# Performance work log

Measured on AMD Instinct MI355X. Metric: run time of the kernel, lower is better.

The kernel has to match this reference:

```python
import jax, jax.numpy as jnp
import numpy as np

PAD = 0
N_SENSE = 3
VOCAB = 100000
OUT_VOCAB = 50000
D = 128
B = 64
MAX_LEN = 512


def setup_inputs() -> dict:
    key = jax.random.key(0)
    ks = jax.random.split(key, 8)
    inputs = jax.random.randint(ks[0], (B, MAX_LEN * N_SENSE), 0, VOCAB, dtype=jnp.int64 if jax.config.jax_enable_x64 else jnp.int32)
    length_weights = jax.random.uniform(ks[1], (B, 1, 1), dtype=jnp.float32, minval=0.1, maxval=1.0)
    word_attn_mask = jax.random.bernoulli(ks[2], 0.1, (B, MAX_LEN))
    embedding = jax.random.normal(ks[3], (VOCAB, D), dtype=jnp.float32) * 0.02
    W_attn = jax.random.normal(ks[4], (1, D), dtype=jnp.float32) * 0.02
    b_attn = jnp.zeros((1,), dtype=jnp.float32)
    W_lin = jax.random.normal(ks[5], (OUT_VOCAB, D), dtype=jnp.float32) * 0.02
    b_lin = jnp.zeros((OUT_VOCAB,), dtype=jnp.float32)
    return {"inputs": inputs, "length_weights": length_weights, "word_attn_mask": word_attn_mask,
            "embedding": embedding, "W_attn": W_attn, "b_attn": b_attn, "W_lin": W_lin, "b_lin": b_lin}


def reference(inputs, length_weights, word_attn_mask, embedding, W_attn, b_attn, W_lin, b_lin):
    Bsz, LS = inputs.shape
    L = LS // N_SENSE
    # padding row contributes zeros (nn.Embedding padding_idx=PAD)
    E = embedding.at[PAD].set(0.0)
    embeds = E[inputs]                                   # [B, L*S, D]
    embeds4 = embeds.reshape(Bsz, L, N_SENSE, -1)
    embed_mean = embeds4.mean(axis=2)                    # [B, L, D]
    # word-level attention: Linear(D,1) -> mask -> softmax over words
    word_imp = jnp.einsum('bld,d->bl', embed_mean, W_attn[0]) + b_attn[0]
    word_imp = jnp.where(word_attn_mask, -jnp.inf, word_imp)
    word_w = jax.nn.softmax(word_imp, axis=-1)           # [B, L]
    context = jnp.einsum('bl,bld->bd', word_w, embed_mean)  # [B, D]
    # sense-level attention: similarity of each sense embedding to context
    sim = jnp.einsum('bnd,bd->bn', embeds, context)      # [B, L*S]
    sense_w = jax.nn.softmax(sim.reshape(Bsz, L, N_SENSE), axis=-1).reshape(Bsz, LS)
    attn_w = length_weights.reshape(Bsz, 1) * sense_w    # scale by 1/length
    attn_w = jnp.where(inputs == PAD, 0.0, attn_w)
    hidden = jnp.einsum('bn,bnd->bd', attn_w, embeds)    # [B, D]
    logits = hidden @ W_lin.T + b_lin                    # [B, OUT_VOCAB]
    return jax.nn.log_softmax(logits, axis=-1)
```

## Files before the change

### kernel.cpp

```cpp
#include <hip/hip_runtime.h>
#include <math.h>

#define B_    64
#define L_    512
#define S_    3
#define D_    128
#define OV_   50000
#define VOC_  100000
#define NBLK_ 782

typedef __attribute__((ext_vector_type(8))) short bf16x8;
typedef __attribute__((ext_vector_type(4))) float f32x4;

__device__ __forceinline__ float waveReduceSum(float v) {
#pragma unroll
    for (int off = 32; off >= 1; off >>= 1) v += __shfl_xor(v, off, 64);
    return v;
}
__device__ __forceinline__ float waveReduceMax(float v) {
#pragma unroll
    for (int off = 32; off >= 1; off >>= 1) v = fmaxf(v, __shfl_xor(v, off, 64));
    return v;
}

__device__ __forceinline__ short f2bf(float f) {
    unsigned int u = __float_as_uint(f);
    return (short)((u + 0x7FFFu + ((u >> 16) & 1u)) >> 16);
}

__global__ __launch_bounds__(256) void prequery_kernel(
    const float* __restrict__ emb, const float* __restrict__ Wa,
    float* __restrict__ P, float* __restrict__ context,
    float* __restrict__ hidden)
{
    const int tid = threadIdx.x;
    if (blockIdx.x < 64 && tid < D_) {
        context[blockIdx.x * D_ + tid] = 0.f;
        hidden[blockIdx.x * D_ + tid]  = 0.f;
    }

    const int lane = tid & 63;
    const int q = lane >> 4;
    const int j = lane & 15;
    const int waveg = blockIdx.x * 4 + (tid >> 6);
    const int nwaves = gridDim.x * 4;

    const float4 wa0 = ((const float4*)Wa)[2 * j];
    const float4 wa1 = ((const float4*)Wa)[2 * j + 1];

    for (int r0 = waveg * 4; r0 < VOC_; r0 += nwaves * 4) {
        const float4* row = (const float4*)(emb + (long)(r0 + q) * D_ + j * 8);
        float4 e0 = row[0], e1 = row[1];
        float s = e0.x * wa0.x + e0.y * wa0.y + e0.z * wa0.z + e0.w * wa0.w
                + e1.x * wa1.x + e1.y * wa1.y + e1.z * wa1.z + e1.w * wa1.w;
#pragma unroll
        for (int off = 8; off >= 1; off >>= 1) s += __shfl_xor(s, off, 64);
        if (j == 0) P[r0 + q] = s;
    }
}

__global__ __launch_bounds__(256) void context_kernel(
    const int* __restrict__ inputs, const int* __restrict__ mask,
    const float* __restrict__ P, const float* __restrict__ ba,
    const float* __restrict__ emb, float* __restrict__ context)
{
    const int b    = blockIdx.x >> 4;
    const int base = (blockIdx.x & 15) * 32;
    const int tid  = threadIdx.x;
    const int wave = tid >> 6, lane = tid & 63;
    const int h = lane >> 5, j = lane & 31;

    __shared__ float s_imp[L_];
    __shared__ float s_red[4];
    __shared__ float s_part[8][D_];

    const int* in_b = inputs + b * (L_ * S_);
    const float babias = ba[0];

#pragma unroll
    for (int half = 0; half < 2; ++half) {
        const int l = tid + half * 256;
        float acc = 0.f;
#pragma unroll
        for (int s = 0; s < S_; ++s) {
            int idx = in_b[l * S_ + s];
            if (idx != 0) acc += P[idx];
        }
        float imp = acc * (1.0f / 3.0f) + babias;
        s_imp[l] = mask[b * L_ + l] ? -INFINITY : imp;
    }
    __syncthreads();

    float v0 = s_imp[tid], v1 = s_imp[tid + 256];
    float m = waveReduceMax(fmaxf(v0, v1));
    if (lane == 0) s_red[wave] = m;
    __syncthreads();
    m = fmaxf(fmaxf(s_red[0], s_red[1]), fmaxf(s_red[2], s_red[3]));
    __syncthreads();
    float p0 = expf(v0 - m), p1 = expf(v1 - m);
    float ssum = waveReduceSum(p0 + p1);
    if (lane == 0) s_red[wave] = ssum;
    __syncthreads();
    float inv = (1.0f / 3.0f) / (s_red[0] + s_red[1] + s_red[2] + s_red[3]);
    s_imp[tid]       = p0 * inv;
    s_imp[tid + 256] = p1 * inv;
    __syncthreads();

    float4 c = make_float4(0.f, 0.f, 0.f, 0.f);
    for (int wp = wave; wp < 16; wp += 4) {
        const int l = base + wp * 2 + h;
        const float w = s_imp[l];
        float4 mm = make_float4(0.f, 0.f, 0.f, 0.f);
#pragma unroll
        for (int s = 0; s < S_; ++s) {
            int idx = in_b[l * S_ + s];
            if (idx != 0) {
                float4 e = ((const float4*)(emb + (long)idx * D_))[j];
                mm.x += e.x; mm.y += e.y; mm.z += e.z; mm.w += e.w;
            }
        }
        c.x += w * mm.x; c.y += w * mm.y; c.z += w * mm.z; c.w += w * mm.w;
    }
    ((float4*)s_part[wave * 2 + h])[j] = c;
    __syncthreads();
    if (tid < D_) {
        float acc = 0.f;
#pragma unroll
        for (int p = 0; p < 8; ++p) acc += s_part[p][tid];
        atomicAdd(&context[b * D_ + tid], acc);
    }
}

__global__ __launch_bounds__(256) void sense_kernel(
    const int* __restrict__ inputs, const float* __restrict__ lwp,
    const float* __restrict__ context, const float* __restrict__ emb,
    float* __restrict__ hidden)
{
    const int b    = blockIdx.x >> 4;
    const int base = (blockIdx.x & 15) * 32;
    const int tid  = threadIdx.x;
    const int wave = tid >> 6, lane = tid & 63;
    const int h = lane >> 5, j = lane & 31;

    __shared__ float s_part[8][D_];

    const int* in_b = inputs + b * (L_ * S_);
    const float lwb = lwp[b];
    const float4 c4 = ((const float4*)(context + b * D_))[j];

    float4 hacc = make_float4(0.f, 0.f, 0.f, 0.f);

    for (int wp = wave; wp < 16; wp += 4) {
        const int l = base + wp * 2 + h;
        float4 e[S_]; int id[S_]; float sim[S_];
#pragma unroll
        for (int s = 0; s < S_; ++s) {
            id[s] = in_b[l * S_ + s];
            if (id[s] != 0) e[s] = ((const float4*)(emb + (long)id[s] * D_))[j];
            else e[s] = make_float4(0.f, 0.f, 0.f, 0.f);
            sim[s] = e[s].x * c4.x + e[s].y * c4.y + e[s].z * c4.z + e[s].w * c4.w;
        }
#pragma unroll
        for (int off = 16; off >= 1; off >>= 1) {
            sim[0] += __shfl_xor(sim[0], off, 64);
            sim[1] += __shfl_xor(sim[1], off, 64);
            sim[2] += __shfl_xor(sim[2], off, 64);
        }
        float e0 = expf(sim[0]), e1 = expf(sim[1]), e2 = expf(sim[2]);
        float f = lwb / (e0 + e1 + e2);
        float w0 = (id[0] != 0) ? e0 * f : 0.f;
        float w1 = (id[1] != 0) ? e1 * f : 0.f;
        float w2 = (id[2] != 0) ? e2 * f : 0.f;
        hacc.x += w0 * e[0].x + w1 * e[1].x + w2 * e[2].x;
        hacc.y += w0 * e[0].y + w1 * e[1].y + w2 * e[2].y;
        hacc.z += w0 * e[0].z + w1 * e[1].z + w2 * e[2].z;
        hacc.w += w0 * e[0].w + w1 * e[1].w + w2 * e[2].w;
    }
    ((float4*)s_part[wave * 2 + h])[j] = hacc;
    __syncthreads();
    if (tid < D_) {
        float acc = 0.f;
#pragma unroll
        for (int p = 0; p < 8; ++p) acc += s_part[p][tid];
        atomicAdd(&hidden[b * D_ + tid], acc);
    }
}

__global__ __launch_bounds__(256) void logits_kernel(
    const float* __restrict__ hidden, const float* __restrict__ Wl,
    const float* __restrict__ bl, float* __restrict__ logits,
    float* __restrict__ pS)
{
    __shared__ short s_hbf[64][136];
    const int tid  = threadIdx.x;
    const int wave = tid >> 6, lane = tid & 63;
    const int m15  = lane & 15, quad = lane >> 4;
    const int v    = blockIdx.x * 64 + wave * 16 + m15;
    const bool valid = (v < OV_);
    const int vc   = valid ? v : (OV_ - 1);

    for (int i = tid; i < 2048; i += 256) {
        float4 x = ((const float4*)hidden)[i];
        const int r = i >> 5;
        const int c = (i & 31) * 4;
        short* dst = &s_hbf[r][c];
        dst[0] = f2bf(x.x); dst[1] = f2bf(x.y);
        dst[2] = f2bf(x.z); dst[3] = f2bf(x.w);
    }
    __syncthreads();

    f32x4 acc[4];
#pragma unroll
    for (int t = 0; t < 4; ++t) acc[t] = (f32x4){0.f, 0.f, 0.f, 0.f};

    const float* wrow = Wl + (long)vc * D_ + quad * 8;
#pragma unroll
    for (int ks = 0; ks < 4; ++ks) {
        float4 x0 = *(const float4*)(wrow + ks * 32);
        float4 x1 = *(const float4*)(wrow + ks * 32 + 4);
        bf16x8 bfr;
        bfr[0] = f2bf(x0.x); bfr[1] = f2bf(x0.y); bfr[2] = f2bf(x0.z); bfr[3] = f2bf(x0.w);
        bfr[4] = f2bf(x1.x); bfr[5] = f2bf(x1.y); bfr[6] = f2bf(x1.z); bfr[7] = f2bf(x1.w);
#pragma unroll
        for (int t = 0; t < 4; ++t) {
            bf16x8 afr = *(const bf16x8*)&s_hbf[t * 16 + m15][ks * 32 + quad * 8];
            acc[t] = __builtin_amdgcn_mfma_f32_16x16x32_bf16(afr, bfr,
                                                             acc[t], 0, 0, 0);
        }
    }

    const float bias = bl[vc];
    if (valid) {
#pragma unroll
        for (int t = 0; t < 4; ++t)
#pragma unroll
            for (int r = 0; r < 4; ++r) {
                const int row = t * 16 + quad * 4 + r;
                logits[(long)row * OV_ + v] = acc[t][r] + bias;
            }
    }

    __shared__ float s_ps[64][4];
#pragma unroll
    for (int t = 0; t < 4; ++t) {
#pragma unroll
        for (int r = 0; r < 4; ++r) {
            float se = valid ? expf(acc[t][r] + bias) : 0.f;
#pragma unroll
            for (int off = 8; off >= 1; off >>= 1) se += __shfl_xor(se, off, 64);
            if (m15 == 0) s_ps[t * 16 + quad * 4 + r][wave] = se;
        }
    }
    __syncthreads();
    if (tid < 64)
        pS[tid * NBLK_ + blockIdx.x] = s_ps[tid][0] + s_ps[tid][1]
                                     + s_ps[tid][2] + s_ps[tid][3];
}

__global__ __launch_bounds__(256) void reducez_kernel(
    const float* __restrict__ pS, float* __restrict__ logZ)
{
    const int b = blockIdx.x;
    const int tid = threadIdx.x;
    const int wave = tid >> 6, lane = tid & 63;
    const float* rs = pS + b * NBLK_;
    __shared__ float s_red[4];

    float s = 0.f;
    for (int i = tid; i < NBLK_; i += 256) s += rs[i];
    s = waveReduceSum(s);
    if (lane == 0) s_red[wave] = s;
    __syncthreads();
    if (tid == 0)
        logZ[b] = logf(s_red[0] + s_red[1] + s_red[2] + s_red[3]);
}

__global__ __launch_bounds__(256) void finalize_kernel(
    const float* __restrict__ logits, const float* __restrict__ logZ,
    float* __restrict__ out)
{
    const long i4 = (long)blockIdx.x * 256 + threadIdx.x;
    const long e  = i4 * 4;
    const int b = (int)(e / OV_);
    const float z = logZ[b];
    float4 x = ((const float4*)logits)[i4];
    x.x -= z; x.y -= z; x.z -= z; x.w -= z;
    ((float4*)out)[i4] = x;
}

extern "C" void kernel_launch(void* const* d_in, const int* in_sizes, int n_in,
                              void* d_out, int out_size, void* d_ws, size_t ws_size,
                              hipStream_t stream) {
    const int*   inputs = (const int*)d_in[0];
    const float* lw     = (const float*)d_in[1];
    const int*   mask   = (const int*)d_in[2];
    const float* emb    = (const float*)d_in[3];
    const float* Wa     = (const float*)d_in[4];
    const float* ba     = (const float*)d_in[5];
    const float* Wl     = (const float*)d_in[6];
    const float* bl     = (const float*)d_in[7];
    float* out = (float*)d_out;

    float* ws = (float*)d_ws;
    float* hidden  = ws;
    float* logZ    = ws + 8192;
    float* logits  = ws + 8256;
    float* P       = logits + (long)B_ * OV_;
    float* context = P + VOC_;
    float* pS      = context + B_ * D_;

    prequery_kernel<<<625, 256, 0, stream>>>(emb, Wa, P, context, hidden);
    context_kernel<<<B_ * 16, 256, 0, stream>>>(inputs, mask, P, ba, emb, context);
    sense_kernel<<<B_ * 16, 256, 0, stream>>>(inputs, lw, context, emb, hidden);
    logits_kernel<<<NBLK_, 256, 0, stream>>>(hidden, Wl, bl, logits, pS);
    reducez_kernel<<<B_, 256, 0, stream>>>(pS, logZ);
    finalize_kernel<<<(B_ * OV_) / (4 * 256), 256, 0, stream>>>(logits, logZ, out);
}
```

Baseline: 161.0 us.

## Fuse attention and logits stages into cooperative kernels with grid sync

```diff
diff --git a/kernel.cpp b/kernel.cpp
--- a/kernel.cpp
+++ b/kernel.cpp
@@ -1,5 +1,8 @@
 #include <hip/hip_runtime.h>
+#include <hip/hip_cooperative_groups.h>
 #include <math.h>
+
+namespace cg = cooperative_groups;
 
 #define B_    64
 #define L_    512
@@ -31,13 +34,14 @@
 __global__ __launch_bounds__(256) void prequery_kernel(
     const float* __restrict__ emb, const float* __restrict__ Wa,
     float* __restrict__ P, float* __restrict__ context,
-    float* __restrict__ hidden)
+    float* __restrict__ hidden, float* __restrict__ rowsum)
 {
     const int tid = threadIdx.x;
     if (blockIdx.x < 64 && tid < D_) {
         context[blockIdx.x * D_ + tid] = 0.f;
         hidden[blockIdx.x * D_ + tid]  = 0.f;
     }
+    if (blockIdx.x == 64 && tid < B_) rowsum[tid] = 0.f;
 
     const int lane = tid & 63;
     const int q = lane >> 4;
@@ -59,6 +63,136 @@
     }
 }
 
+__device__ __forceinline__ void word_softmax(
+    const int* in_b, const int* __restrict__ mask, const float* __restrict__ P,
+    float babias, int b, float* s_imp, float* s_red)
+{
+    const int tid = threadIdx.x;
+    const int wave = tid >> 6, lane = tid & 63;
+#pragma unroll
+    for (int half = 0; half < 2; ++half) {
+        const int l = tid + half * 256;
+        float acc = 0.f;
+#pragma unroll
+        for (int s = 0; s < S_; ++s) {
+            int idx = in_b[l * S_ + s];
+            if (idx != 0) acc += P[idx];
+        }
+        float imp = acc * (1.0f / 3.0f) + babias;
+        s_imp[l] = mask[b * L_ + l] ? -INFINITY : imp;
+    }
+    __syncthreads();
+
+    float v0 = s_imp[tid], v1 = s_imp[tid + 256];
+    float m = waveReduceMax(fmaxf(v0, v1));
+    if (lane == 0) s_red[wave] = m;
+    __syncthreads();
+    m = fmaxf(fmaxf(s_red[0], s_red[1]), fmaxf(s_red[2], s_red[3]));
+    __syncthreads();
+    float p0 = expf(v0 - m), p1 = expf(v1 - m);
+    float ssum = waveReduceSum(p0 + p1);
+    if (lane == 0) s_red[wave] = ssum;
+    __syncthreads();
+    float inv = (1.0f / 3.0f) / (s_red[0] + s_red[1] + s_red[2] + s_red[3]);
+    s_imp[tid]       = p0 * inv;
+    s_imp[tid + 256] = p1 * inv;
+    __syncthreads();
+}
+
+__global__ __launch_bounds__(256, 2) void attn_fused(
+    const int* __restrict__ inputs, const int* __restrict__ mask,
+    const float* __restrict__ P, const float* __restrict__ ba,
+    const float* __restrict__ emb, const float* __restrict__ lwp,
+    float* __restrict__ context, float* __restrict__ hidden)
+{
+    cg::grid_group grid = cg::this_grid();
+
+    const int b    = blockIdx.x >> 3;
+    const int base = (blockIdx.x & 7) * 64;
+    const int tid  = threadIdx.x;
+    const int wave = tid >> 6, lane = tid & 63;
+    const int h = lane >> 5, j = lane & 31;
+
+    __shared__ float s_imp[L_];
+    __shared__ float s_red[4];
+    __shared__ float s_part[8][D_];
+
+    const int* in_b = inputs + b * (L_ * S_);
+    word_softmax(in_b, mask, P, ba[0], b, s_imp, s_red);
+
+    float4 ereg[8][3];
+    int    pmask[8];
+    float4 c = make_float4(0.f, 0.f, 0.f, 0.f);
+#pragma unroll
+    for (int it = 0; it < 8; ++it) {
+        const int l = base + (wave + it * 4) * 2 + h;
+        const float w = s_imp[l];
+        int pm = 0;
+        float4 mm = make_float4(0.f, 0.f, 0.f, 0.f);
+#pragma unroll
+        for (int s = 0; s < S_; ++s) {
+            int idx = in_b[l * S_ + s];
+            float4 e = make_float4(0.f, 0.f, 0.f, 0.f);
+            if (idx != 0) {
+                e = ((const float4*)(emb + (long)idx * D_))[j];
+                pm |= (1 << s);
+            }
+            ereg[it][s] = e;
+            mm.x += e.x; mm.y += e.y; mm.z += e.z; mm.w += e.w;
+        }
+        pmask[it] = pm;
+        c.x += w * mm.x; c.y += w * mm.y; c.z += w * mm.z; c.w += w * mm.w;
+    }
+    ((float4*)s_part[wave * 2 + h])[j] = c;
+    __syncthreads();
+    if (tid < D_) {
+        float acc = 0.f;
+#pragma unroll
+        for (int p = 0; p < 8; ++p) acc += s_part[p][tid];
+        atomicAdd(&context[b * D_ + tid], acc);
+    }
+
+    grid.sync();
+
+    const float lwb = lwp[b];
+    const float4 c4 = ((const float4*)(context + b * D_))[j];
+
+    float4 hacc = make_float4(0.f, 0.f, 0.f, 0.f);
+#pragma unroll
+    for (int it = 0; it < 8; ++it) {
+        float sim[S_];
+#pragma unroll
+        for (int s = 0; s < S_; ++s) {
+            float4 e = ereg[it][s];
+            sim[s] = e.x * c4.x + e.y * c4.y + e.z * c4.z + e.w * c4.w;
+        }
+#pragma unroll
+        for (int off = 16; off >= 1; off >>= 1) {
+            sim[0] += __shfl_xor(sim[0], off, 64);
+            sim[1] += __shfl_xor(sim[1], off, 64);
+            sim[2] += __shfl_xor(sim[2], off, 64);
+        }
+        float e0 = expf(sim[0]), e1 = expf(sim[1]), e2 = expf(sim[2]);
+        float f = lwb / (e0 + e1 + e2);
+        float w0 = (pmask[it] & 1) ? e0 * f : 0.f;
+        float w1 = (pmask[it] & 2) ? e1 * f : 0.f;
+        float w2 = (pmask[it] & 4) ? e2 * f : 0.f;
+        hacc.x += w0 * ereg[it][0].x + w1 * ereg[it][1].x + w2 * ereg[it][2].x;
+        hacc.y += w0 * ereg[it][0].y + w1 * ereg[it][1].y + w2 * ereg[it][2].y;
+        hacc.z += w0 * ereg[it][0].z + w1 * ereg[it][1].z + w2 * ereg[it][2].z;
+        hacc.w += w0 * ereg[it][0].w + w1 * ereg[it][1].w + w2 * ereg[it][2].w;
+    }
+    __syncthreads();
+    ((float4*)s_part[wave * 2 + h])[j] = hacc;
+    __syncthreads();
+    if (tid < D_) {
+        float acc = 0.f;
+#pragma unroll
+        for (int p = 0; p < 8; ++p) acc += s_part[p][tid];
+        atomicAdd(&hidden[b * D_ + tid], acc);
+    }
+}
+
 __global__ __launch_bounds__(256) void context_kernel(
     const int* __restrict__ inputs, const int* __restrict__ mask,
     const float* __restrict__ P, const float* __restrict__ ba,
@@ -75,36 +209,7 @@
     __shared__ float s_part[8][D_];
 
     const int* in_b = inputs + b * (L_ * S_);
-    const float babias = ba[0];
-
-#pragma unroll
-    for (int half = 0; half < 2; ++half) {
-        const int l = tid + half * 256;
-        float acc = 0.f;
-#pragma unroll
-        for (int s = 0; s < S_; ++s) {
-            int idx = in_b[l * S_ + s];
-            if (idx != 0) acc += P[idx];
-        }
-        float imp = acc * (1.0f / 3.0f) + babias;
-        s_imp[l] = mask[b * L_ + l] ? -INFINITY : imp;
-    }
-    __syncthreads();
-
-    float v0 = s_imp[tid], v1 = s_imp[tid + 256];
-    float m = waveReduceMax(fmaxf(v0, v1));
-    if (lane == 0) s_red[wave] = m;
-    __syncthreads();
-    m = fmaxf(fmaxf(s_red[0], s_red[1]), fmaxf(s_red[2], s_red[3]));
-    __syncthreads();
-    float p0 = expf(v0 - m), p1 = expf(v1 - m);
-    float ssum = waveReduceSum(p0 + p1);
-    if (lane == 0) s_red[wave] = ssum;
-    __syncthreads();
-    float inv = (1.0f / 3.0f) / (s_red[0] + s_red[1] + s_red[2] + s_red[3]);
-    s_imp[tid]       = p0 * inv;
-    s_imp[tid + 256] = p1 * inv;
-    __syncthreads();
+    word_softmax(in_b, mask, P, ba[0], b, s_imp, s_red);
 
     float4 c = make_float4(0.f, 0.f, 0.f, 0.f);
     for (int wp = wave; wp < 16; wp += 4) {
@@ -149,7 +254,6 @@
     const float4 c4 = ((const float4*)(context + b * D_))[j];
 
     float4 hacc = make_float4(0.f, 0.f, 0.f, 0.f);
-
     for (int wp = wave; wp < 16; wp += 4) {
         const int l = base + wp * 2 + h;
         float4 e[S_]; int id[S_]; float sim[S_];
@@ -186,18 +290,20 @@
     }
 }
 
-__global__ __launch_bounds__(256) void logits_kernel(
+__global__ __launch_bounds__(256, 2) void logits_fused(
     const float* __restrict__ hidden, const float* __restrict__ Wl,
-    const float* __restrict__ bl, float* __restrict__ logits,
-    float* __restrict__ pS)
-{
+    const float* __restrict__ bl, float* __restrict__ rowsum,
+    float* __restrict__ out)
+{
+    cg::grid_group grid = cg::this_grid();
+
     __shared__ short s_hbf[64][136];
+    __shared__ float s_ps[64][4];
+    __shared__ float s_logz[64];
+
     const int tid  = threadIdx.x;
     const int wave = tid >> 6, lane = tid & 63;
     const int m15  = lane & 15, quad = lane >> 4;
-    const int v    = blockIdx.x * 64 + wave * 16 + m15;
-    const bool valid = (v < OV_);
-    const int vc   = valid ? v : (OV_ - 1);
 
     for (int i = tid; i < 2048; i += 256) {
         float4 x = ((const float4*)hidden)[i];
@@ -209,6 +315,90 @@
     }
     __syncthreads();
 
+    int  v[2];   bool valid[2];  float bias[2];
+    f32x4 acc[2][4];
+#pragma unroll
+    for (int tl = 0; tl < 2; ++tl) {
+        v[tl] = blockIdx.x * 128 + tl * 64 + wave * 16 + m15;
+        valid[tl] = (v[tl] < OV_);
+        const int vc = valid[tl] ? v[tl] : (OV_ - 1);
+        bias[tl] = bl[vc];
+#pragma unroll
+        for (int t = 0; t < 4; ++t) acc[tl][t] = (f32x4){0.f, 0.f, 0.f, 0.f};
+        const float* wrow = Wl + (long)vc * D_ + quad * 8;
+#pragma unroll
+        for (int ks = 0; ks < 4; ++ks) {
+            float4 x0 = *(const float4*)(wrow + ks * 32);
+            float4 x1 = *(const float4*)(wrow + ks * 32 + 4);
+            bf16x8 bfr;
+            bfr[0] = f2bf(x0.x); bfr[1] = f2bf(x0.y); bfr[2] = f2bf(x0.z); bfr[3] = f2bf(x0.w);
+            bfr[4] = f2bf(x1.x); bfr[5] = f2bf(x1.y); bfr[6] = f2bf(x1.z); bfr[7] = f2bf(x1.w);
+#pragma unroll
+            for (int t = 0; t < 4; ++t) {
+                bf16x8 afr = *(const bf16x8*)&s_hbf[t * 16 + m15][ks * 32 + quad * 8];
+                acc[tl][t] = __builtin_amdgcn_mfma_f32_16x16x32_bf16(afr, bfr,
+                                                                     acc[tl][t], 0, 0, 0);
+            }
+        }
+    }
+
+#pragma unroll
+    for (int t = 0; t < 4; ++t) {
+#pragma unroll
+        for (int r = 0; r < 4; ++r) {
+            float se = (valid[0] ? expf(acc[0][t][r] + bias[0]) : 0.f)
+                     + (valid[1] ? expf(acc[1][t][r] + bias[1]) : 0.f);
+#pragma unroll
+            for (int off = 8; off >= 1; off >>= 1) se += __shfl_xor(se, off, 64);
+            if (m15 == 0) s_ps[t * 16 + quad * 4 + r][wave] = se;
+        }
+    }
+    __syncthreads();
+    if (tid < 64)
+        atomicAdd(&rowsum[tid],
+                  s_ps[tid][0] + s_ps[tid][1] + s_ps[tid][2] + s_ps[tid][3]);
+
+    grid.sync();
+
+    if (tid < 64) s_logz[tid] = logf(rowsum[tid]);
+    __syncthreads();
+
+#pragma unroll
+    for (int tl = 0; tl < 2; ++tl) {
+        if (!valid[tl]) continue;
+#pragma unroll
+        for (int t = 0; t < 4; ++t)
+#pragma unroll
+            for (int r = 0; r < 4; ++r) {
+                const int row = t * 16 + quad * 4 + r;
+                out[(long)row * OV_ + v[tl]] = acc[tl][t][r] + bias[tl] - s_logz[row];
+            }
+    }
+}
+
+__global__ __launch_bounds__(256) void logits_kernel(
+    const float* __restrict__ hidden, const float* __restrict__ Wl,
+    const float* __restrict__ bl, float* __restrict__ logits,
+    float* __restrict__ pS)
+{
+    __shared__ short s_hbf[64][136];
+    const int tid  = threadIdx.x;
+    const int wave = tid >> 6, lane = tid & 63;
+    const int m15  = lane & 15, quad = lane >> 4;
+    const int v    = blockIdx.x * 64 + wave * 16 + m15;
+    const bool valid = (v < OV_);
+    const int vc   = valid ? v : (OV_ - 1);
+
+    for (int i = tid; i < 2048; i += 256) {
+        float4 x = ((const float4*)hidden)[i];
+        const int r = i >> 5;
+        const int c = (i & 31) * 4;
+        short* dst = &s_hbf[r][c];
+        dst[0] = f2bf(x.x); dst[1] = f2bf(x.y);
+        dst[2] = f2bf(x.z); dst[3] = f2bf(x.w);
+    }
+    __syncthreads();
+
     f32x4 acc[4];
 #pragma unroll
     for (int t = 0; t < 4; ++t) acc[t] = (f32x4){0.f, 0.f, 0.f, 0.f};
@@ -228,7 +418,6 @@
                                                              acc[t], 0, 0, 0);
         }
     }
-
     const float bias = bl[vc];
     if (valid) {
 #pragma unroll
@@ -303,16 +492,42 @@
 
     float* ws = (float*)d_ws;
     float* hidden  = ws;
-    float* logZ    = ws + 8192;
-    float* logits  = ws + 8256;
-    float* P       = logits + (long)B_ * OV_;
-    float* context = P + VOC_;
-    float* pS      = context + B_ * D_;
-
-    prequery_kernel<<<625, 256, 0, stream>>>(emb, Wa, P, context, hidden);
-    context_kernel<<<B_ * 16, 256, 0, stream>>>(inputs, mask, P, ba, emb, context);
-    sense_kernel<<<B_ * 16, 256, 0, stream>>>(inputs, lw, context, emb, hidden);
-    logits_kernel<<<NBLK_, 256, 0, stream>>>(hidden, Wl, bl, logits, pS);
-    reducez_kernel<<<B_, 256, 0, stream>>>(pS, logZ);
-    finalize_kernel<<<(B_ * OV_) / (4 * 256), 256, 0, stream>>>(logits, logZ, out);
-}
+    float* context = ws + 8192;
+    float* rowsum  = ws + 16384;
+    float* logZ    = ws + 16448;
+    float* P       = ws + 16512;
+    float* logits  = ws + 116512;
+    float* pS      = logits + (long)B_ * OV_;
+
+    prequery_kernel<<<625, 256, 0, stream>>>(emb, Wa, P, context, hidden, rowsum);
+
+    {
+        void* args[] = { (void*)&inputs, (void*)&mask, (void*)&P, (void*)&ba,
+                         (void*)&emb, (void*)&lw, (void*)&context, (void*)&hidden };
+        hipError_t e = hipLaunchCooperativeKernel((void*)attn_fused,
+                                                  dim3(B_ * 8), dim3(256),
+                                                  args, 0, stream);
+        if (e != hipSuccess) {
+            (void)hipGetLastError();
+            context_kernel<<<B_ * 16, 256, 0, stream>>>(inputs, mask, P, ba,
+                                                        emb, context);
+            sense_kernel<<<B_ * 16, 256, 0, stream>>>(inputs, lw, context, emb,
+                                                      hidden);
+        }
+    }
+
+    {
+        void* args[] = { (void*)&hidden, (void*)&Wl, (void*)&bl,
+                         (void*)&rowsum, (void*)&out };
+        hipError_t e = hipLaunchCooperativeKernel((void*)logits_fused,
+                                                  dim3(391), dim3(256),
+                                                  args, 0, stream);
+        if (e != hipSuccess) {
+            (void)hipGetLastError();
+            logits_kernel<<<NBLK_, 256, 0, stream>>>(hidden, Wl, bl, logits, pS);
+            reducez_kernel<<<B_, 256, 0, stream>>>(pS, logZ);
+            finalize_kernel<<<(B_ * OV_) / (4 * 256), 256, 0, stream>>>(logits,
+                                                                        logZ, out);
+        }
+    }
+}
```

After: 261.0 us. +62.1%, slower.

## Fuse logZ reduction into finalize and split sense kernel across more blocks

Applied to the files above, without the earlier changes.

```diff
diff --git a/kernel.cpp b/kernel.cpp
--- a/kernel.cpp
+++ b/kernel.cpp
@@ -59,6 +59,42 @@
     }
 }
 
+__device__ __forceinline__ void word_softmax(
+    const int* in_b, const int* __restrict__ mask, const float* __restrict__ P,
+    float babias, int b, float* s_imp, float* s_red)
+{
+    const int tid = threadIdx.x;
+    const int wave = tid >> 6, lane = tid & 63;
+#pragma unroll
+    for (int half = 0; half < 2; ++half) {
+        const int l = tid + half * 256;
+        float acc = 0.f;
+#pragma unroll
+        for (int s = 0; s < S_; ++s) {
+            int idx = in_b[l * S_ + s];
+            if (idx != 0) acc += P[idx];
+        }
+        float imp = acc * (1.0f / 3.0f) + babias;
+        s_imp[l] = mask[b * L_ + l] ? -INFINITY : imp;
+    }
+    __syncthreads();
+
+    float v0 = s_imp[tid], v1 = s_imp[tid + 256];
+    float m = waveReduceMax(fmaxf(v0, v1));
+    if (lane == 0) s_red[wave] = m;
+    __syncthreads();
+    m = fmaxf(fmaxf(s_red[0], s_red[1]), fmaxf(s_red[2], s_red[3]));
+    __syncthreads();
+    float p0 = expf(v0 - m), p1 = expf(v1 - m);
+    float ssum = waveReduceSum(p0 + p1);
+    if (lane == 0) s_red[wave] = ssum;
+    __syncthreads();
+    float inv = (1.0f / 3.0f) / (s_red[0] + s_red[1] + s_red[2] + s_red[3]);
+    s_imp[tid]       = p0 * inv;
+    s_imp[tid + 256] = p1 * inv;
+    __syncthreads();
+}
+
 __global__ __launch_bounds__(256) void context_kernel(
     const int* __restrict__ inputs, const int* __restrict__ mask,
     const float* __restrict__ P, const float* __restrict__ ba,
@@ -75,36 +111,7 @@
     __shared__ float s_part[8][D_];
 
     const int* in_b = inputs + b * (L_ * S_);
-    const float babias = ba[0];
-
-#pragma unroll
-    for (int half = 0; half < 2; ++half) {
-        const int l = tid + half * 256;
-        float acc = 0.f;
-#pragma unroll
-        for (int s = 0; s < S_; ++s) {
-            int idx = in_b[l * S_ + s];
-            if (idx != 0) acc += P[idx];
-        }
-        float imp = acc * (1.0f / 3.0f) + babias;
-        s_imp[l] = mask[b * L_ + l] ? -INFINITY : imp;
-    }
-    __syncthreads();
-
-    float v0 = s_imp[tid], v1 = s_imp[tid + 256];
-    float m = waveReduceMax(fmaxf(v0, v1));
-    if (lane == 0) s_red[wave] = m;
-    __syncthreads();
-    m = fmaxf(fmaxf(s_red[0], s_red[1]), fmaxf(s_red[2], s_red[3]));
-    __syncthreads();
-    float p0 = expf(v0 - m), p1 = expf(v1 - m);
-    float ssum = waveReduceSum(p0 + p1);
-    if (lane == 0) s_red[wave] = ssum;
-    __syncthreads();
-    float inv = (1.0f / 3.0f) / (s_red[0] + s_red[1] + s_red[2] + s_red[3]);
-    s_imp[tid]       = p0 * inv;
-    s_imp[tid + 256] = p1 * inv;
-    __syncthreads();
+    word_softmax(in_b, mask, P, ba[0], b, s_imp, s_red);
 
     float4 c = make_float4(0.f, 0.f, 0.f, 0.f);
     for (int wp = wave; wp < 16; wp += 4) {
@@ -136,8 +143,8 @@
     const float* __restrict__ context, const float* __restrict__ emb,
     float* __restrict__ hidden)
 {
-    const int b    = blockIdx.x >> 4;
-    const int base = (blockIdx.x & 15) * 32;
+    const int b    = blockIdx.x >> 5;
+    const int base = (blockIdx.x & 31) * 16;
     const int tid  = threadIdx.x;
     const int wave = tid >> 6, lane = tid & 63;
     const int h = lane >> 5, j = lane & 31;
@@ -149,8 +156,7 @@
     const float4 c4 = ((const float4*)(context + b * D_))[j];
 
     float4 hacc = make_float4(0.f, 0.f, 0.f, 0.f);
-
-    for (int wp = wave; wp < 16; wp += 4) {
+    for (int wp = wave; wp < 8; wp += 4) {
         const int l = base + wp * 2 + h;
         float4 e[S_]; int id[S_]; float sim[S_];
 #pragma unroll
@@ -228,7 +234,6 @@
                                                              acc[t], 0, 0, 0);
         }
     }
-
     const float bias = bl[vc];
     if (valid) {
 #pragma unroll
@@ -257,35 +262,34 @@
                                      + s_ps[tid][2] + s_ps[tid][3];
 }
 
-__global__ __launch_bounds__(256) void reducez_kernel(
-    const float* __restrict__ pS, float* __restrict__ logZ)
-{
-    const int b = blockIdx.x;
-    const int tid = threadIdx.x;
-    const int wave = tid >> 6, lane = tid & 63;
+__global__ __launch_bounds__(256) void finalize_kernel(
+    const float* __restrict__ logits, const float* __restrict__ pS,
+    float* __restrict__ out)
+{
+    const int b     = blockIdx.x / 49;
+    const int chunk = blockIdx.x % 49;
+    const int tid   = threadIdx.x;
+    const int wave  = tid >> 6, lane = tid & 63;
+
+    __shared__ float s_red[4];
+    __shared__ float s_logz;
+
     const float* rs = pS + b * NBLK_;
-    __shared__ float s_red[4];
-
     float s = 0.f;
     for (int i = tid; i < NBLK_; i += 256) s += rs[i];
     s = waveReduceSum(s);
     if (lane == 0) s_red[wave] = s;
     __syncthreads();
-    if (tid == 0)
-        logZ[b] = logf(s_red[0] + s_red[1] + s_red[2] + s_red[3]);
-}
-
-__global__ __launch_bounds__(256) void finalize_kernel(
-    const float* __restrict__ logits, const float* __restrict__ logZ,
-    float* __restrict__ out)
-{
-    const long i4 = (long)blockIdx.x * 256 + threadIdx.x;
-    const long e  = i4 * 4;
-    const int b = (int)(e / OV_);
-    const float z = logZ[b];
-    float4 x = ((const float4*)logits)[i4];
-    x.x -= z; x.y -= z; x.z -= z; x.w -= z;
-    ((float4*)out)[i4] = x;
+    if (tid == 0) s_logz = logf(s_red[0] + s_red[1] + s_red[2] + s_red[3]);
+    __syncthreads();
+    const float z = s_logz;
+
+    const int i4 = chunk * 256 + tid;
+    if (i4 < OV_ / 4) {
+        float4 x = ((const float4*)(logits + (long)b * OV_))[i4];
+        x.x -= z; x.y -= z; x.z -= z; x.w -= z;
+        ((float4*)(out + (long)b * OV_))[i4] = x;
+    }
 }
 
 extern "C" void kernel_launch(void* const* d_in, const int* in_sizes, int n_in,
@@ -303,16 +307,14 @@
 
     float* ws = (float*)d_ws;
     float* hidden  = ws;
-    float* logZ    = ws + 8192;
-    float* logits  = ws + 8256;
-    float* P       = logits + (long)B_ * OV_;
-    float* context = P + VOC_;
-    float* pS      = context + B_ * D_;
+    float* context = ws + 8192;
+    float* P       = ws + 16384;
+    float* logits  = ws + 116384 + 96;
+    float* pS      = logits + (long)B_ * OV_;
 
     prequery_kernel<<<625, 256, 0, stream>>>(emb, Wa, P, context, hidden);
     context_kernel<<<B_ * 16, 256, 0, stream>>>(inputs, mask, P, ba, emb, context);
-    sense_kernel<<<B_ * 16, 256, 0, stream>>>(inputs, lw, context, emb, hidden);
+    sense_kernel<<<B_ * 32, 256, 0, stream>>>(inputs, lw, context, emb, hidden);
     logits_kernel<<<NBLK_, 256, 0, stream>>>(hidden, Wl, bl, logits, pS);
-    reducez_kernel<<<B_, 256, 0, stream>>>(pS, logZ);
-    finalize_kernel<<<(B_ * OV_) / (4 * 256), 256, 0, stream>>>(logits, logZ, out);
-}
+    finalize_kernel<<<B_ * 49, 256, 0, stream>>>(logits, pS, out);
+}
```

Result: no change. 162.1 us (+0.6%).
